# Kernel optimization log

Hardware: AMD Instinct MI355X
Metric: run time of the kernel (lower is better)

The kernel has to match this reference:

```python
import jax, jax.numpy as jnp
import numpy as np

B, S, V, E, H, M, OOV = 64, 400, 50000, 128, 512, 512, 20


def setup_inputs() -> dict:
    key = jax.random.key(0)
    ks = jax.random.split(key, 24)
    d = {}
    d["y"] = jax.random.randint(ks[0], (B,), 0, V)
    d["h"] = jax.random.normal(ks[1], (1, B, H), jnp.float32)
    d["memory_bank"] = jax.random.normal(ks[2], (B, S, M), jnp.float32)
    d["src_mask"] = jnp.ones((B, S), jnp.float32)
    d["max_num_oovs"] = OOV
    d["src_oov"] = jax.random.randint(ks[3], (B, S), 0, V + OOV)
    d["coverage"] = jax.random.uniform(ks[4], (B, S), jnp.float32)
    # parameters (torch Linear convention: W [out, in])
    sc = 0.02
    d["emb_W"] = jax.random.normal(ks[5], (V, E), jnp.float32) * sc
    d["gru_W_ih"] = jax.random.normal(ks[6], (3 * H, E), jnp.float32) * sc
    d["gru_W_hh"] = jax.random.normal(ks[7], (3 * H, H), jnp.float32) * sc
    d["gru_b_ih"] = jnp.zeros((3 * H,), jnp.float32)
    d["gru_b_hh"] = jnp.zeros((3 * H,), jnp.float32)
    d["attn_Wm"] = jax.random.normal(ks[8], (H, M), jnp.float32) * sc
    d["attn_Wd"] = jax.random.normal(ks[9], (H, H), jnp.float32) * sc
    d["attn_bd"] = jnp.zeros((H,), jnp.float32)
    d["attn_Wc"] = jax.random.normal(ks[10], (H, 1), jnp.float32) * sc
    d["attn_v"] = jax.random.normal(ks[11], (H,), jnp.float32) * sc
    d["pgen_W"] = jax.random.normal(ks[12], (1, E + H + M), jnp.float32) * sc
    d["pgen_b"] = jnp.zeros((1,), jnp.float32)
    d["vd1_W"] = jax.random.normal(ks[13], (H, H + M), jnp.float32) * sc
    d["vd1_b"] = jnp.zeros((H,), jnp.float32)
    d["vd2_W"] = jax.random.normal(ks[14], (V, H), jnp.float32) * sc
    d["vd2_b"] = jnp.zeros((V,), jnp.float32)
    return d


def _decode_step(y, h, memory_bank, src_mask, max_num_oovs, src_oov, coverage,
                 emb_W, gru_W_ih, gru_W_hh, gru_b_ih, gru_b_hh,
                 attn_Wm, attn_Wd, attn_bd, attn_Wc, attn_v,
                 pgen_W, pgen_b, vd1_W, vd1_b, vd2_W, vd2_b):
    bsz = src_oov.shape[0]
    y_emb = emb_W[y]                                   # [B,E]
    # --- single-step GRU (num_layers=1, torch gate layout r,z,n) ---
    h0 = h[0]                                          # [B,H]
    gi = y_emb @ gru_W_ih.T + gru_b_ih                 # [B,3H]
    gh = h0 @ gru_W_hh.T + gru_b_hh                    # [B,3H]
    i_r, i_z, i_n = jnp.split(gi, 3, axis=-1)
    h_r, h_z, h_n = jnp.split(gh, 3, axis=-1)
    r = jax.nn.sigmoid(i_r + h_r)
    z = jax.nn.sigmoid(i_z + h_z)
    n = jnp.tanh(i_n + r * h_n)
    h1 = (1.0 - z) * n + z * h0                        # [B,H]
    h_next = h1[None]                                  # [1,B,H]
    # --- additive (concat) attention with coverage ---
    enc_feat = memory_bank @ attn_Wm.T                 # [B,S,H]
    dec_feat = h1 @ attn_Wd.T + attn_bd                # [B,H]
    cov_feat = coverage[..., None] * attn_Wc[:, 0]     # [B,S,H]
    scores = jnp.tanh(enc_feat + dec_feat[:, None, :] + cov_feat) @ attn_v  # [B,S]
    scores = jnp.where(src_mask > 0, scores, -1e9)
    attn = jax.nn.softmax(scores, axis=1) * src_mask
    attn = attn / (attn.sum(axis=1, keepdims=True) + 1e-10)  # masked softmax
    word_context = jnp.einsum('bs,bsm->bm', attn, memory_bank)
    coverage_next = coverage + attn
    # --- vocab distribution ---
    vocab_in = jnp.concatenate([word_context, h1], axis=1)   # [B,M+H]
    hid = vocab_in @ vd1_W.T + vd1_b
    vocab_dist = jax.nn.softmax(hid @ vd2_W.T + vd2_b, axis=1)  # [B,V]
    # --- pointer-generator merge ---
    pgen_in = jnp.concatenate([word_context, h1, y_emb], axis=1)
    p_gen = jax.nn.sigmoid(pgen_in @ pgen_W.T + pgen_b)      # [B,1]
    vocab_dist_ = p_gen * vocab_dist
    attn_dist_ = (1.0 - p_gen) * attn
    if max_num_oovs > 0:
        vocab_dist_ = jnp.concatenate(
            [vocab_dist_, jnp.zeros((bsz, max_num_oovs), vocab_dist_.dtype)], axis=1)
    rows = jnp.arange(bsz)[:, None]
    final_dist = vocab_dist_.at[rows, src_oov].add(attn_dist_)  # [B,V+OOV]
    return final_dist, h_next, word_context, attn, p_gen, coverage_next


def reference(y, h, memory_bank, src_mask, max_num_oovs, src_oov, coverage,
              emb_W, gru_W_ih, gru_W_hh, gru_b_ih, gru_b_hh,
              attn_Wm, attn_Wd, attn_bd, attn_Wc, attn_v,
              pgen_W, pgen_b, vd1_W, vd1_b, vd2_W, vd2_b):
    return _decode_step(y, h, memory_bank, src_mask, max_num_oovs, src_oov, coverage,
                        emb_W, gru_W_ih, gru_W_hh, gru_b_ih, gru_b_hh,
                        attn_Wm, attn_Wd, attn_bd, attn_Wc, attn_v,
                        pgen_W, pgen_b, vd1_W, vd1_b, vd2_W, vd2_b)
```

## Files before the change

kernel.cpp:

```cpp
#include <hip/hip_runtime.h>

typedef unsigned short u16;
typedef unsigned int u32;
using bf16x8 = __attribute__((ext_vector_type(8))) short;
using f32x4  = __attribute__((ext_vector_type(4))) float;

#define B_ 64
#define S_ 400
#define E_ 128
#define H_ 512
#define M_ 512
#define R_ (B_ * S_)

__device__ __forceinline__ float b2f(u16 u){
  union { u32 i; float f; } c; c.i = ((u32)u) << 16; return c.f;
}
__device__ __forceinline__ u16 f2b(float f){
  union { u32 i; float f; } c; c.f = f;
  u32 r = c.i + 0x7FFFu + ((c.i >> 16) & 1u);
  return (u16)(r >> 16);
}
__device__ __forceinline__ float sigm(float x){ return 1.0f / (1.0f + __expf(-x)); }
__device__ __forceinline__ float fast_tanh(float x){
  float e = __expf(2.0f * x);
  return 1.0f - 2.0f / (e + 1.0f);
}
__device__ __forceinline__ bf16x8 pack8(const float* __restrict__ p){
  const u32* u = (const u32*)p;
  union { u32 w[4]; bf16x8 v; } c;
  c.w[0] = (u[1] & 0xFFFF0000u) | (u[0] >> 16);
  c.w[1] = (u[3] & 0xFFFF0000u) | (u[2] >> 16);
  c.w[2] = (u[5] & 0xFFFF0000u) | (u[4] >> 16);
  c.w[3] = (u[7] & 0xFFFF0000u) | (u[6] >> 16);
  return c.v;
}
__device__ __forceinline__ bf16x8 pack8r(float4 a, float4 b){
  union { u32 w[4]; bf16x8 v; } c;
  c.w[0] = (__float_as_uint(a.y) & 0xFFFF0000u) | (__float_as_uint(a.x) >> 16);
  c.w[1] = (__float_as_uint(a.w) & 0xFFFF0000u) | (__float_as_uint(a.z) >> 16);
  c.w[2] = (__float_as_uint(b.y) & 0xFFFF0000u) | (__float_as_uint(b.x) >> 16);
  c.w[3] = (__float_as_uint(b.w) & 0xFFFF0000u) | (__float_as_uint(b.z) >> 16);
  return c.v;
}

__global__ void k0_zero(float* __restrict__ scores, float* __restrict__ ctx_ws,
                        float* __restrict__ yemb_ws,
                        const int* __restrict__ y, const float* __restrict__ embW,
                        const float* __restrict__ Wm, u16* __restrict__ wmbf){
  int i = blockIdx.x * 256 + threadIdx.x;
  if (i < R_) { scores[i] = 0.f; return; }
  i -= R_;
  if (i < B_ * M_) { ctx_ws[i] = 0.f; return; }
  i -= B_ * M_;
  if (i < B_ * E_) {
    int b = i >> 7, e = i & 127;
    yemb_ws[i] = embW[(size_t)y[b] * E_ + e];
    return;
  }
  i -= B_ * E_;
  if (i < (H_ * M_) / 8) {
    int j16 = i >> 10;
    int rem = i & 1023;
    int ks  = rem >> 6;
    int l   = rem & 63;
    int row = j16 * 16 + (l & 15);
    int col = ks * 32 + (l >> 4) * 8;
    *(bf16x8*)(wmbf + (size_t)i * 8) = pack8(Wm + (size_t)row * 512 + col);
  }
}

__global__ __launch_bounds__(256) void k1a_gru(
    const float* __restrict__ h, const float* __restrict__ yemb_ws,
    const float* __restrict__ Wih, const float* __restrict__ Whh,
    const float* __restrict__ bih, const float* __restrict__ bhh,
    float* __restrict__ h1_ws, float* __restrict__ h_out)
{
  __shared__ float red_r[4][64], red_z[4][64], red_nh[4][64], red_ni[4][64];
  int hh = blockIdx.x;
  int t = threadIdx.x, w = t >> 6, lane = t & 63;
  const float* xrow = h + lane * H_;
  const float* erow = yemb_ws + lane * E_;
  const float* wr = Whh + (size_t)hh * H_;
  const float* wz = Whh + (size_t)(hh + H_) * H_;
  const float* wn = Whh + (size_t)(hh + 2 * H_) * H_;
  float pr = 0.f, pz = 0.f, pnh = 0.f, pni = 0.f;
  int k0 = w * 128;
  #pragma unroll 8
  for (int k = k0; k < k0 + 128; k += 4){
    float4 x = *(const float4*)(xrow + k);
    float4 a = *(const float4*)(wr + k);
    float4 bq = *(const float4*)(wz + k);
    float4 c = *(const float4*)(wn + k);
    pr  += a.x*x.x + a.y*x.y + a.z*x.z + a.w*x.w;
    pz  += bq.x*x.x + bq.y*x.y + bq.z*x.z + bq.w*x.w;
    pnh += c.x*x.x + c.y*x.y + c.z*x.z + c.w*x.w;
  }
  const float* ur = Wih + (size_t)hh * E_;
  const float* uz = Wih + (size_t)(hh + H_) * E_;
  const float* un = Wih + (size_t)(hh + 2 * H_) * E_;
  int e0 = w * 32;
  #pragma unroll
  for (int k = e0; k < e0 + 32; k += 4){
    float4 x = *(const float4*)(erow + k);
    float4 a = *(const float4*)(ur + k);
    float4 bq = *(const float4*)(uz + k);
    float4 c = *(const float4*)(un + k);
    pr  += a.x*x.x + a.y*x.y + a.z*x.z + a.w*x.w;
    pz  += bq.x*x.x + bq.y*x.y + bq.z*x.z + bq.w*x.w;
    pni += c.x*x.x + c.y*x.y + c.z*x.z + c.w*x.w;
  }
  red_r[w][lane] = pr; red_z[w][lane] = pz;
  red_nh[w][lane] = pnh; red_ni[w][lane] = pni;
  __syncthreads();
  if (t < 64){
    int b = t;
    float rr = bih[hh] + bhh[hh];
    float zz = bih[H_ + hh] + bhh[H_ + hh];
    float nh = bhh[2 * H_ + hh];
    float ni = bih[2 * H_ + hh];
    #pragma unroll
    for (int ww = 0; ww < 4; ww++){
      rr += red_r[ww][b]; zz += red_z[ww][b];
      nh += red_nh[ww][b]; ni += red_ni[ww][b];
    }
    float r = sigm(rr), z = sigm(zz);
    float n = fast_tanh(ni + r * nh);
    float h0v = h[b * H_ + hh];
    float h1v = (1.0f - z) * n + z * h0v;
    h1_ws[b * H_ + hh] = h1v;
    h_out[b * H_ + hh] = h1v;
  }
}

__global__ __launch_bounds__(256) void k1b_dec(
    const float* __restrict__ h1_ws, const float* __restrict__ Wd,
    const float* __restrict__ bd, float* __restrict__ dec_ws)
{
  __shared__ float red[4][64];
  int hh = blockIdx.x;
  int t = threadIdx.x, w = t >> 6, lane = t & 63;
  const float* xrow = h1_ws + lane * H_;
  const float* wd = Wd + (size_t)hh * H_;
  float p = 0.f;
  int k0 = w * 128;
  #pragma unroll 8
  for (int k = k0; k < k0 + 128; k += 4){
    float4 x = *(const float4*)(xrow + k);
    float4 a = *(const float4*)(wd + k);
    p += a.x*x.x + a.y*x.y + a.z*x.z + a.w*x.w;
  }
  red[w][lane] = p;
  __syncthreads();
  if (t < 64){
    float s = bd[hh] + red[0][t] + red[1][t] + red[2][t] + red[3][t];
    dec_ws[t * H_ + hh] = s;
  }
}

__global__ __launch_bounds__(512) void k2_scores(
    const float* __restrict__ mb, const u16* __restrict__ wmbf,
    const float* __restrict__ dec, const float* __restrict__ cov,
    const float* __restrict__ Wc, const float* __restrict__ av,
    float* __restrict__ scores)
{
  __shared__ u16 alds[2][32 * 128];
  int t = threadIdx.x;
  int lane = t & 63, w = t >> 6;
  int quad = lane >> 4, l16 = lane & 15;
  int rowB = blockIdx.x * 32;
  int cb = w * 64;
  f32x4 acc[2][4];
  #pragma unroll
  for (int rg = 0; rg < 2; rg++)
    #pragma unroll
    for (int j = 0; j < 4; j++) acc[rg][j] = (f32x4){0.f,0.f,0.f,0.f};

  int srow = t >> 4, sg8 = t & 15;
  int sw0 = srow * 128 + 8 * (sg8 ^ (srow & 7));
  {
    const float* g0 = mb + (size_t)(rowB + srow) * 512 + sg8 * 8;
    float4 a0 = *(const float4*)g0, b0 = *(const float4*)(g0 + 4);
    *(bf16x8*)&alds[0][sw0] = pack8r(a0, b0);
  }
  const u16* wlane = wmbf + lane * 8;
  bf16x8 bcur[4];
  #pragma unroll
  for (int j = 0; j < 4; j++)
    bcur[j] = *(const bf16x8*)(wlane + (size_t)((w * 4 + j) * 16) * 512);
  __syncthreads();
  for (int c = 0; c < 4; c++){
    float4 pa0, pb0;
    if (c < 3){
      const float* g0 = mb + (size_t)(rowB + srow) * 512 + (c + 1) * 128 + sg8 * 8;
      pa0 = *(const float4*)g0; pb0 = *(const float4*)(g0 + 4);
    }
    const u16* buf = alds[c & 1];
    #pragma unroll
    for (int s = 0; s < 4; s++){
      bf16x8 bnxt[4];
      bool more = (s < 3) || (c < 3);
      if (more){
        int kn = c * 4 + s + 1;
        #pragma unroll
        for (int j = 0; j < 4; j++)
          bnxt[j] = *(const bf16x8*)(wlane + (size_t)((w * 4 + j) * 16 + kn) * 512);
      }
      bf16x8 af[2];
      #pragma unroll
      for (int rg = 0; rg < 2; rg++)
        af[rg] = *(const bf16x8*)&buf[(rg * 16 + l16) * 128 + 8 * ((s * 4 + quad) ^ (l16 & 7))];
      #pragma unroll
      for (int j = 0; j < 4; j++)
        #pragma unroll
        for (int rg = 0; rg < 2; rg++)
          acc[rg][j] = __builtin_amdgcn_mfma_f32_16x16x32_bf16(af[rg], bcur[j], acc[rg][j], 0, 0, 0);
      if (more){
        #pragma unroll
        for (int j = 0; j < 4; j++) bcur[j] = bnxt[j];
      }
    }
    if (c < 3){
      u16* d = (u16*)alds[(c + 1) & 1];
      *(bf16x8*)&d[sw0] = pack8r(pa0, pb0);
    }
    __syncthreads();
  }
  float vv[4], wcv[4];
  #pragma unroll
  for (int j = 0; j < 4; j++){
    int hc = cb + j * 16 + l16;
    vv[j] = av[hc]; wcv[j] = Wc[hc];
  }
  #pragma unroll
  for (int rg = 0; rg < 2; rg++){
    #pragma unroll
    for (int r = 0; r < 4; r++){
      int R = rowB + rg * 16 + quad * 4 + r;
      int bb = R / S_;
      float cf = cov[R];
      const float* decb = dec + bb * H_;
      float sum = 0.f;
      #pragma unroll
      for (int j = 0; j < 4; j++){
        int hc = cb + j * 16 + l16;
        float e = acc[rg][j][r] + decb[hc] + cf * wcv[j];
        sum += fast_tanh(e) * vv[j];
      }
      #pragma unroll
      for (int m = 1; m < 16; m <<= 1) sum += __shfl_xor(sum, m, 64);
      if (l16 == 0) atomicAdd(&scores[R], sum);
    }
  }
}

__global__ __launch_bounds__(256) void k3a_softmax(
    const float* __restrict__ scores, const float* __restrict__ mask,
    const float* __restrict__ cov,
    float* __restrict__ attn_ws,
    float* __restrict__ out_attn, float* __restrict__ out_cov)
{
  __shared__ float p_s[S_];
  __shared__ float m_s[S_];
  __shared__ float red[256];
  int b = blockIdx.x, t = threadIdx.x;
  float lmax = -3.0e38f;
  for (int s = t; s < S_; s += 256){
    float mk = mask[b*S_ + s];
    float v = scores[b*S_ + s];
    v = (mk > 0.f) ? v : -1e9f;
    p_s[s] = v; m_s[s] = mk;
    lmax = fmaxf(lmax, v);
  }
  red[t] = lmax; __syncthreads();
  for (int o = 128; o > 0; o >>= 1){ if (t < o) red[t] = fmaxf(red[t], red[t+o]); __syncthreads(); }
  float MX = red[0]; __syncthreads();
  float lsum = 0.f;
  for (int s = t; s < S_; s += 256){ float e = __expf(p_s[s] - MX); p_s[s] = e; lsum += e; }
  red[t] = lsum; __syncthreads();
  for (int o = 128; o > 0; o >>= 1){ if (t < o) red[t] += red[t+o]; __syncthreads(); }
  float inv1 = 1.0f / red[0]; __syncthreads();
  float l2 = 0.f;
  for (int s = t; s < S_; s += 256){ float a = p_s[s] * inv1 * m_s[s]; p_s[s] = a; l2 += a; }
  red[t] = l2; __syncthreads();
  for (int o = 128; o > 0; o >>= 1){ if (t < o) red[t] += red[t+o]; __syncthreads(); }
  float inv2 = 1.0f / (red[0] + 1e-10f); __syncthreads();
  for (int s = t; s < S_; s += 256){
    float a = p_s[s] * inv2;
    attn_ws[b*S_ + s] = a;
    out_attn[b*S_ + s] = a;
    out_cov[b*S_ + s]  = cov[b*S_ + s] + a;
  }
}

__global__ __launch_bounds__(256) void k3b_ctx(
    const float* __restrict__ attn_ws, const float* __restrict__ mb,
    float* __restrict__ ctx_ws)
{
  int b = blockIdx.x, sc = blockIdx.y, t = threadIdx.x;
  int m0 = t * 2;
  const float* mbb = mb + (size_t)b * S_ * M_;
  const float* ab  = attn_ws + b * S_;
  float a0 = 0.f, a1 = 0.f;
  int s0 = sc * 25;
  for (int s = s0; s < s0 + 25; s++){
    float a = ab[s];
    float2 c = *(const float2*)(mbb + s*M_ + m0);
    a0 += a * c.x;
    a1 += a * c.y;
  }
  atomicAdd(&ctx_ws[b*M_ + m0],     a0);
  atomicAdd(&ctx_ws[b*M_ + m0 + 1], a1);
}

__global__ __launch_bounds__(512) void k4_hid_pgen(
    const float* __restrict__ ctx_ws, const float* __restrict__ h1_ws,
    const float* __restrict__ yemb_ws,
    const float* __restrict__ vd1W, const float* __restrict__ vd1b,
    const float* __restrict__ pgW,  const float* __restrict__ pgb,
    u16* __restrict__ hid_bf, float* __restrict__ pgen_ws, float* __restrict__ out_pgen,
    float* __restrict__ out_ctx)
{
  __shared__ float vin[1024];
  __shared__ float red[512];
  int b = blockIdx.x, t = threadIdx.x;
  for (int i = t; i < 1024; i += 512){
    if (i < 512){
      float c = ctx_ws[b*512 + i];
      vin[i] = c;
      out_ctx[b*512 + i] = c;
    } else {
      vin[i] = h1_ws[b*512 + (i - 512)];
    }
  }
  __syncthreads();
  int hh = t;
  float acc = vd1b[hh];
  const float* wrow = vd1W + (size_t)hh * 1024;
  for (int k = 0; k < 1024; k += 4){
    float4 c = *(const float4*)(wrow + k);
    acc += c.x*vin[k] + c.y*vin[k+1] + c.z*vin[k+2] + c.w*vin[k+3];
  }
  hid_bf[b*512 + hh] = f2b(acc);
  float p = 0.f;
  for (int i = t; i < 1152; i += 512){
    float x = (i < 1024) ? vin[i] : yemb_ws[b*128 + (i - 1024)];
    p += x * pgW[i];
  }
  red[t] = p; __syncthreads();
  for (int o = 256; o > 0; o >>= 1){ if (t < o) red[t] += red[t+o]; __syncthreads(); }
  if (t == 0){
    float pg = sigm(red[0] + pgb[0]);
    pgen_ws[b] = pg; out_pgen[b] = pg;
  }
}

__global__ __launch_bounds__(256) void k5_logits(
    const u16* __restrict__ hid_bf, const float* __restrict__ vd2W,
    const float* __restrict__ vd2b, int V, u16* __restrict__ logits_bf)
{
  __shared__ u16 blds[2][64 * 128];
  int t = threadIdx.x;
  int lane = t & 63, w = t >> 6;
  int quad = lane >> 4, l16 = lane & 15;
  int cb = blockIdx.x * 64;
  f32x4 acc[4];
  #pragma unroll
  for (int rg = 0; rg < 4; rg++) acc[rg] = (f32x4){0.f,0.f,0.f,0.f};

  int scol0 = t >> 4, sg8 = t & 15;
  {
    #pragma unroll
    for (int i = 0; i < 4; i++){
      int col = scol0 + i * 16;
      int gr = cb + col; if (gr > V - 1) gr = V - 1;
      const float* gs = vd2W + (size_t)gr * 512 + sg8 * 8;
      float4 x = *(const float4*)gs, yv = *(const float4*)(gs + 4);
      *(bf16x8*)&blds[0][col * 128 + 8 * (sg8 ^ (col & 7))] = pack8r(x, yv);
    }
  }
  __syncthreads();
  int cw = w * 16 + l16;
  for (int c = 0; c < 4; c++){
    float4 px0, py0, px1, py1, px2, py2, px3, py3;
    if (c < 3){
      int kc = (c + 1) * 128;
      int g0 = cb + scol0;      if (g0 > V-1) g0 = V-1;
      int g1 = cb + scol0 + 16; if (g1 > V-1) g1 = V-1;
      int g2 = cb + scol0 + 32; if (g2 > V-1) g2 = V-1;
      int g3 = cb + scol0 + 48; if (g3 > V-1) g3 = V-1;
      const float* s0 = vd2W + (size_t)g0 * 512 + kc + sg8 * 8;
      const float* s1 = vd2W + (size_t)g1 * 512 + kc + sg8 * 8;
      const float* s2 = vd2W + (size_t)g2 * 512 + kc + sg8 * 8;
      const float* s3 = vd2W + (size_t)g3 * 512 + kc + sg8 * 8;
      px0 = *(const float4*)s0; py0 = *(const float4*)(s0 + 4);
      px1 = *(const float4*)s1; py1 = *(const float4*)(s1 + 4);
      px2 = *(const float4*)s2; py2 = *(const float4*)(s2 + 4);
      px3 = *(const float4*)s3; py3 = *(const float4*)(s3 + 4);
    }
    bf16x8 aF[4][4];
    #pragma unroll
    for (int s = 0; s < 4; s++)
      #pragma unroll
      for (int rg = 0; rg < 4; rg++)
        aF[s][rg] = *(const bf16x8*)(hid_bf + (size_t)(rg * 16 + l16) * 512 + c * 128 + s * 32 + quad * 8);
    const u16* buf = blds[c & 1];
    #pragma unroll
    for (int s = 0; s < 4; s++){
      bf16x8 bfb = *(const bf16x8*)&buf[cw * 128 + 8 * ((s * 4 + quad) ^ (cw & 7))];
      #pragma unroll
      for (int rg = 0; rg < 4; rg++)
        acc[rg] = __builtin_amdgcn_mfma_f32_16x16x32_bf16(aF[s][rg], bfb, acc[rg], 0, 0, 0);
    }
    if (c < 3){
      u16* d = (u16*)blds[(c + 1) & 1];
      *(bf16x8*)&d[scol0 * 128        + 8 * (sg8 ^ (scol0 & 7))]        = pack8r(px0, py0);
      *(bf16x8*)&d[(scol0+16) * 128   + 8 * (sg8 ^ ((scol0+16) & 7))]   = pack8r(px1, py1);
      *(bf16x8*)&d[(scol0+32) * 128   + 8 * (sg8 ^ ((scol0+32) & 7))]   = pack8r(px2, py2);
      *(bf16x8*)&d[(scol0+48) * 128   + 8 * (sg8 ^ ((scol0+48) & 7))]   = pack8r(px3, py3);
    }
    __syncthreads();
  }
  int v = cb + w * 16 + l16;
  if (v < V){
    float bias = vd2b[v];
    #pragma unroll
    for (int rg = 0; rg < 4; rg++){
      #pragma unroll
      for (int r = 0; r < 4; r++){
        int bb = rg * 16 + quad * 4 + r;
        logits_bf[(size_t)bb * V + v] = f2b(acc[rg][r] + bias);
      }
    }
  }
}

__global__ __launch_bounds__(256) void k6a_partial(
    const u16* __restrict__ logits_bf, int V,
    float* __restrict__ mxp, float* __restrict__ denp)
{
  __shared__ float red[256];
  int b = blockIdx.x, ch = blockIdx.y, t = threadIdx.x;
  int VG = V >> 3;
  int per = (VG + 7) >> 3;
  int g0 = ch * per;
  int g1 = g0 + per; if (g1 > VG) g1 = VG;
  const bf16x8* row = (const bf16x8*)(logits_bf + (size_t)b * V);
  float x[32];
  float m = -3.0e38f;
  #pragma unroll
  for (int i = 0; i < 4; i++){
    int g = g0 + t + i * 256;
    bool ok = g < g1;
    bf16x8 v;
    if (ok) v = row[g];
    #pragma unroll
    for (int j = 0; j < 8; j++){
      float f = ok ? b2f((u16)v[j]) : -3.0e38f;
      x[i * 8 + j] = f;
      m = fmaxf(m, f);
    }
  }
  red[t] = m; __syncthreads();
  for (int o = 128; o > 0; o >>= 1){ if (t < o) red[t] = fmaxf(red[t], red[t+o]); __syncthreads(); }
  float MX = red[0]; __syncthreads();
  float s = 0.f;
  #pragma unroll
  for (int k = 0; k < 32; k++) s += __expf(x[k] - MX);
  red[t] = s; __syncthreads();
  for (int o = 128; o > 0; o >>= 1){ if (t < o) red[t] += red[t+o]; __syncthreads(); }
  if (t == 0){ mxp[b * 8 + ch] = MX; denp[b * 8 + ch] = red[0]; }
}

__global__ void k6b_combine(const float* __restrict__ mxp, const float* __restrict__ denp,
                            float* __restrict__ mx_ws, float* __restrict__ den_ws)
{
  int b = threadIdx.x;
  float M = -3.0e38f;
  #pragma unroll
  for (int c = 0; c < 8; c++) M = fmaxf(M, mxp[b * 8 + c]);
  float d = 0.f;
  #pragma unroll
  for (int c = 0; c < 8; c++) d += denp[b * 8 + c] * __expf(mxp[b * 8 + c] - M);
  mx_ws[b] = M; den_ws[b] = d;
}

__global__ void k7a_vocab(const u16* __restrict__ logits_bf,
    const float* __restrict__ mx_ws, const float* __restrict__ den_ws,
    const float* __restrict__ pgen_ws, int V, int VO, float* __restrict__ out_final)
{
  int b = blockIdx.y;
  int c = (blockIdx.x * 256 + threadIdx.x) * 4;
  if (c >= VO) return;
  float MX = mx_ws[b];
  float inv = pgen_ws[b] / den_ws[b];
  float v4[4] = {0.f, 0.f, 0.f, 0.f};
  if (c + 3 < V){
    ushort4 u = *(const ushort4*)(logits_bf + (size_t)b * V + c);
    v4[0] = inv * __expf(b2f(u.x) - MX);
    v4[1] = inv * __expf(b2f(u.y) - MX);
    v4[2] = inv * __expf(b2f(u.z) - MX);
    v4[3] = inv * __expf(b2f(u.w) - MX);
  } else {
    #pragma unroll
    for (int j = 0; j < 4; j++){
      int cc = c + j;
      if (cc < V) v4[j] = inv * __expf(b2f(logits_bf[(size_t)b * V + cc]) - MX);
    }
  }
  if (c + 4 <= VO){
    *(float4*)(out_final + (size_t)b * VO + c) = make_float4(v4[0], v4[1], v4[2], v4[3]);
  } else {
    for (int j = 0; j < 4 && c + j < VO; j++) out_final[(size_t)b * VO + c + j] = v4[j];
  }
}

__global__ void k7b_scatter(const int* __restrict__ src_oov,
    const float* __restrict__ attn_ws, const float* __restrict__ pgen_ws,
    int VO, float* __restrict__ out_final)
{
  int idx = blockIdx.x * 256 + threadIdx.x;
  if (idx >= R_) return;
  int b = idx / S_;
  float ad = (1.0f - pgen_ws[b]) * attn_ws[idx];
  atomicAdd(&out_final[(size_t)b*VO + src_oov[idx]], ad);
}

extern "C" void kernel_launch(void* const* d_in, const int* in_sizes, int n_in,
                              void* d_out, int out_size, void* d_ws, size_t ws_size,
                              hipStream_t stream)
{
  const int*   y      = (const int*)d_in[0];
  const float* h      = (const float*)d_in[1];
  const float* mb     = (const float*)d_in[2];
  const float* mask   = (const float*)d_in[3];
  const int*   srcoov = (const int*)d_in[5];
  const float* cov    = (const float*)d_in[6];
  const float* embW   = (const float*)d_in[7];
  const float* Wih    = (const float*)d_in[8];
  const float* Whh    = (const float*)d_in[9];
  const float* bih    = (const float*)d_in[10];
  const float* bhh    = (const float*)d_in[11];
  const float* Wm     = (const float*)d_in[12];
  const float* Wd     = (const float*)d_in[13];
  const float* bd     = (const float*)d_in[14];
  const float* Wc     = (const float*)d_in[15];
  const float* av     = (const float*)d_in[16];
  const float* pgW    = (const float*)d_in[17];
  const float* pgb    = (const float*)d_in[18];
  const float* vd1W   = (const float*)d_in[19];
  const float* vd1b   = (const float*)d_in[20];
  const float* vd2W   = (const float*)d_in[21];
  const float* vd2b   = (const float*)d_in[22];

  const int V  = in_sizes[22];
  const int VO = (int)((long long)out_size / B_ - (H_ + M_ + 2*S_ + 1));

  float* out = (float*)d_out;
  float* out_final = out;
  float* out_h     = out_final + (size_t)B_ * VO;
  float* out_ctx   = out_h     + (size_t)B_ * H_;
  float* out_attn  = out_ctx   + (size_t)B_ * M_;
  float* out_pgen  = out_attn  + (size_t)B_ * S_;
  float* out_cov   = out_pgen  + B_;

  float* ws      = (float*)d_ws;
  float* scores  = ws;
  float* h1_ws   = ws + 25600;
  float* yemb_ws = ws + 58368;
  float* dec_ws  = ws + 66560;
  float* attn_ws = ws + 99328;
  float* ctx_ws  = ws + 124928;
  float* pgen_ws = ws + 157696;
  float* mx_ws   = ws + 157760;
  float* den_ws  = ws + 157824;
  u16*   hid_bf    = (u16*)(ws + 157888);
  u16*   logits_bf = (u16*)(ws + 174272);
  u16*   wm_bf     = logits_bf;
  float* mxp_ws  = scores;
  float* denp_ws = scores + 512;

  hipLaunchKernelGGL(k0_zero,    dim3(388),  dim3(256), 0, stream,
                     scores, ctx_ws, yemb_ws, y, embW, Wm, wm_bf);
  hipLaunchKernelGGL(k1a_gru,    dim3(512),  dim3(256), 0, stream,
                     h, yemb_ws, Wih, Whh, bih, bhh, h1_ws, out_h);
  hipLaunchKernelGGL(k1b_dec,    dim3(512),  dim3(256), 0, stream,
                     h1_ws, Wd, bd, dec_ws);
  hipLaunchKernelGGL(k2_scores,  dim3(800),  dim3(512), 0, stream,
                     mb, wm_bf, dec_ws, cov, Wc, av, scores);
  hipLaunchKernelGGL(k3a_softmax, dim3(64),  dim3(256), 0, stream,
                     scores, mask, cov, attn_ws, out_attn, out_cov);
  hipLaunchKernelGGL(k3b_ctx,    dim3(64, 16), dim3(256), 0, stream,
                     attn_ws, mb, ctx_ws);
  hipLaunchKernelGGL(k4_hid_pgen, dim3(64),  dim3(512), 0, stream,
                     ctx_ws, h1_ws, yemb_ws, vd1W, vd1b, pgW, pgb, hid_bf, pgen_ws, out_pgen, out_ctx);
  hipLaunchKernelGGL(k5_logits,  dim3((V + 63) / 64), dim3(256), 0, stream,
                     hid_bf, vd2W, vd2b, V, logits_bf);
  hipLaunchKernelGGL(k6a_partial, dim3(64, 8), dim3(256), 0, stream,
                     logits_bf, V, mxp_ws, denp_ws);
  hipLaunchKernelGGL(k6b_combine, dim3(1),   dim3(64), 0, stream,
                     mxp_ws, denp_ws, mx_ws, den_ws);
  hipLaunchKernelGGL(k7a_vocab,  dim3((VO + 1023) / 1024, 64), dim3(256), 0, stream,
                     logits_bf, mx_ws, den_ws, pgen_ws, V, VO, out_final);
  hipLaunchKernelGGL(k7b_scatter, dim3(100), dim3(256), 0, stream,
                     srcoov, attn_ws, pgen_ws, VO, out_final);
}
```

Before: 421.7 us.

## Split hidden projection and p_gen into separate kernels with output-row parallelism

The fused per-batch kernel that computed the vd1 hidden projection and p_gen is split in two. The hidden projection now launches one block per output row (512 blocks), with four waves each covering a quarter of K for all 64 batch rows and combining partial sums through shared memory. This reads each vd1 weight row once instead of once per batch block and spreads the work over many more CUs than the old 64 blocks. p_gen and the context copy move to a small separate kernel, which costs one extra launch, and hid_bf is written with a strided pattern.

```diff
diff --git a/kernel.cpp b/kernel.cpp
--- a/kernel.cpp
+++ b/kernel.cpp
@@ -312,46 +312,57 @@
   atomicAdd(&ctx_ws[b*M_ + m0 + 1], a1);
 }
 
-__global__ __launch_bounds__(512) void k4_hid_pgen(
+__global__ __launch_bounds__(256) void k4a_hid(
+    const float* __restrict__ ctx_ws, const float* __restrict__ h1_ws,
+    const float* __restrict__ vd1W, const float* __restrict__ vd1b,
+    u16* __restrict__ hid_bf)
+{
+  __shared__ float red[4][64];
+  int hh = blockIdx.x;
+  int t = threadIdx.x, w = t >> 6, lane = t & 63;
+  int k0 = w * 256;
+  const float* xbase = (w < 2) ? (ctx_ws + lane * 512 + k0)
+                               : (h1_ws + lane * 512 + (k0 - 512));
+  const float* wrow = vd1W + (size_t)hh * 1024 + k0;
+  float p = 0.f;
+  #pragma unroll 8
+  for (int k = 0; k < 256; k += 4){
+    float4 x = *(const float4*)(xbase + k);
+    float4 a = *(const float4*)(wrow + k);
+    p += a.x*x.x + a.y*x.y + a.z*x.z + a.w*x.w;
+  }
+  red[w][lane] = p;
+  __syncthreads();
+  if (t < 64){
+    float s = vd1b[hh] + red[0][t] + red[1][t] + red[2][t] + red[3][t];
+    hid_bf[t * 512 + hh] = f2b(s);
+  }
+}
+
+__global__ __launch_bounds__(128) void k4b_pgen(
     const float* __restrict__ ctx_ws, const float* __restrict__ h1_ws,
     const float* __restrict__ yemb_ws,
-    const float* __restrict__ vd1W, const float* __restrict__ vd1b,
-    const float* __restrict__ pgW,  const float* __restrict__ pgb,
-    u16* __restrict__ hid_bf, float* __restrict__ pgen_ws, float* __restrict__ out_pgen,
+    const float* __restrict__ pgW, const float* __restrict__ pgb,
+    float* __restrict__ pgen_ws, float* __restrict__ out_pgen,
     float* __restrict__ out_ctx)
 {
-  __shared__ float vin[1024];
-  __shared__ float red[512];
+  __shared__ float red[128];
   int b = blockIdx.x, t = threadIdx.x;
-  for (int i = t; i < 1024; i += 512){
-    if (i < 512){
-      float c = ctx_ws[b*512 + i];
-      vin[i] = c;
-      out_ctx[b*512 + i] = c;
-    } else {
-      vin[i] = h1_ws[b*512 + (i - 512)];
-    }
-  }
-  __syncthreads();
-  int hh = t;
-  float acc = vd1b[hh];
-  const float* wrow = vd1W + (size_t)hh * 1024;
-  for (int k = 0; k < 1024; k += 4){
-    float4 c = *(const float4*)(wrow + k);
-    acc += c.x*vin[k] + c.y*vin[k+1] + c.z*vin[k+2] + c.w*vin[k+3];
-  }
-  hid_bf[b*512 + hh] = f2b(acc);
   float p = 0.f;
-  for (int i = t; i < 1152; i += 512){
-    float x = (i < 1024) ? vin[i] : yemb_ws[b*128 + (i - 1024)];
+  for (int i = t; i < 1152; i += 128){
+    float x = (i < 512) ? ctx_ws[b * 512 + i]
+            : (i < 1024) ? h1_ws[b * 512 + (i - 512)]
+                         : yemb_ws[b * 128 + (i - 1024)];
     p += x * pgW[i];
   }
   red[t] = p; __syncthreads();
-  for (int o = 256; o > 0; o >>= 1){ if (t < o) red[t] += red[t+o]; __syncthreads(); }
+  for (int o = 64; o > 0; o >>= 1){ if (t < o) red[t] += red[t + o]; __syncthreads(); }
   if (t == 0){
     float pg = sigm(red[0] + pgb[0]);
     pgen_ws[b] = pg; out_pgen[b] = pg;
   }
+  for (int i = t; i < 512; i += 128)
+    out_ctx[b * 512 + i] = ctx_ws[b * 512 + i];
 }
 
 __global__ __launch_bounds__(256) void k5_logits(
@@ -591,8 +602,10 @@
                      scores, mask, cov, attn_ws, out_attn, out_cov);
   hipLaunchKernelGGL(k3b_ctx,    dim3(64, 16), dim3(256), 0, stream,
                      attn_ws, mb, ctx_ws);
-  hipLaunchKernelGGL(k4_hid_pgen, dim3(64),  dim3(512), 0, stream,
-                     ctx_ws, h1_ws, yemb_ws, vd1W, vd1b, pgW, pgb, hid_bf, pgen_ws, out_pgen, out_ctx);
+  hipLaunchKernelGGL(k4a_hid,    dim3(512),  dim3(256), 0, stream,
+                     ctx_ws, h1_ws, vd1W, vd1b, hid_bf);
+  hipLaunchKernelGGL(k4b_pgen,   dim3(64),   dim3(128), 0, stream,
+                     ctx_ws, h1_ws, yemb_ws, pgW, pgb, pgen_ws, out_pgen, out_ctx);
   hipLaunchKernelGGL(k5_logits,  dim3((V + 63) / 64), dim3(256), 0, stream,
                      hid_bf, vd2W, vd2b, V, logits_bf);
   hipLaunchKernelGGL(k6a_partial, dim3(64, 8), dim3(256), 0, stream,
```

Measured after the change: 390.7 us. -7.3%, faster.
